# Kernel tuning notes

Measured on AMD Instinct MI355X. Metric: run time of the kernel, lower is better.

## Reference

```python
import jax, jax.numpy as jnp
import numpy as np

NEG_SLOPE = 0.2


def gat_conv(x, src, dst, W, a_src, a_dst, b, heads, out_ch, concat):
    """PyG-style GATConv (eval mode, self-loops already appended to src/dst)."""
    N = x.shape[0]
    h = (x @ W).reshape(N, heads, out_ch)            # [N,H,C]
    alpha_s = jnp.einsum('nhc,hc->nh', h, a_src)     # [N,H]
    alpha_d = jnp.einsum('nhc,hc->nh', h, a_dst)
    e = jax.nn.leaky_relu(alpha_s[src] + alpha_d[dst], NEG_SLOPE)  # [E,H]
    # segment softmax over incoming edges per destination node
    m = jax.ops.segment_max(e, dst, num_segments=N)  # every node has a self loop
    ex = jnp.exp(e - m[dst])
    denom = jax.ops.segment_sum(ex, dst, num_segments=N)
    alpha = ex / (denom[dst] + 1e-16)                # [E,H]
    msg = h[src] * alpha[:, :, None]                 # [E,H,C]
    out = jax.ops.segment_sum(msg, dst, num_segments=N)  # [N,H,C]
    if concat:
        out = out.reshape(N, heads * out_ch)
    else:
        out = out.mean(axis=1)
    return out + b


def setup_inputs() -> dict:
    key = jax.random.key(0)
    ks = jax.random.split(key, 12)
    N, E, F_IN = 100000, 3200000, 512
    H1, C1 = 8, 8           # conv1: heads=8, out=8, concat -> 64
    H2, C2 = 8, 16          # conv2: heads=8, out=num_classes=16, mean over heads
    x = jax.random.normal(ks[0], (N, F_IN), dtype=jnp.float32)
    edge_index = jax.random.randint(ks[1], (2, E), 0, N, dtype=jnp.int32)
    g = lambda k, s, fan: jax.random.normal(k, s, dtype=jnp.float32) / np.sqrt(fan)
    return {
        'x': x,
        'edge_index': edge_index,
        'W1': g(ks[2], (F_IN, H1 * C1), F_IN),
        'a_src1': g(ks[3], (H1, C1), C1),
        'a_dst1': g(ks[4], (H1, C1), C1),
        'b1': jnp.zeros((H1 * C1,), jnp.float32),
        'W2': g(ks[5], (H1 * C1, H2 * C2), H1 * C1),
        'a_src2': g(ks[6], (H2, C2), C2),
        'a_dst2': g(ks[7], (H2, C2), C2),
        'b2': jnp.zeros((C2,), jnp.float32),
    }


def reference(x, edge_index, W1, a_src1, a_dst1, b1, W2, a_src2, a_dst2, b2):
    N = x.shape[0]
    loops = jnp.arange(N, dtype=edge_index.dtype)
    src = jnp.concatenate([edge_index[0], loops])
    dst = jnp.concatenate([edge_index[1], loops])
    h = gat_conv(x, src, dst, W1, a_src1, a_dst1, b1, heads=8, out_ch=8, concat=True)
    h = jax.nn.elu(h)
    out = gat_conv(h, src, dst, W2, a_src2, a_dst2, b2, heads=8, out_ch=16, concat=False)
    return out
```

## Files before the change

kernel.cpp:

```cpp
#include <hip/hip_runtime.h>
#include <hip/hip_bf16.h>
#include <hip/hip_fp16.h>
#include <cstddef>

#define NEG_SLOPE 0.2f

typedef _Float16 half8 __attribute__((ext_vector_type(8)));
typedef float floatx4 __attribute__((ext_vector_type(4)));
typedef float floatx2 __attribute__((ext_vector_type(2)));


__global__ __launch_bounds__(256) void pre_k(const int* __restrict__ dst, int E,
                                             int* __restrict__ bhist, int* __restrict__ bh_blocks,
                                             int NB,
                                             const float* __restrict__ W1, _Float16* __restrict__ W1T,
                                             const float* __restrict__ W2, _Float16* __restrict__ W2T) {
    int b = blockIdx.x;
    if (b < 512) {
        __shared__ int lh[256];
        for (int t = threadIdx.x; t < 256; t += 256) lh[t] = 0;
        __syncthreads();
        int per = (E + 511) / 512;
        int s = b * per;
        int e = min(s + per, E);
        for (int i = s + threadIdx.x; i < e; i += 256) atomicAdd(&lh[dst[i] >> 9], 1);
        __syncthreads();
        for (int t = threadIdx.x; t < 256; t += 256) {
            int c = lh[t];
            bh_blocks[b * 256 + t] = c;
            if (c && t < NB) atomicAdd(&bhist[t], c);
        }
    } else if (b < 640) {
        int i = (b - 512) * 256 + threadIdx.x;
        if (i < 512 * 64) {
            int k = i / 64, n = i % 64;
            W1T[(size_t)n * 512 + k] = (_Float16)W1[i];
        }
    } else {
        int i = (b - 640) * 256 + threadIdx.x;
        if (i < 64 * 128) {
            int k = i / 128, n = i % 128;
            W2T[(size_t)n * 64 + k] = (_Float16)W2[i];
        }
    }
}

__global__ __launch_bounds__(256) void bucket_scan_k(const int* __restrict__ bhist, int NB,
                                                     int* __restrict__ bbase,
                                                     int* __restrict__ row_start, int N, int E) {
    __shared__ int tmp[256];
    int tid = threadIdx.x;
    int v = (tid < NB) ? bhist[tid] : 0;
    tmp[tid] = v;
    __syncthreads();
    for (int d = 1; d < 256; d <<= 1) {
        int t = tmp[tid];
        int a = (tid >= d) ? tmp[tid - d] : 0;
        __syncthreads();
        tmp[tid] = t + a;
        __syncthreads();
    }
    if (tid < NB) {
        bbase[tid] = tmp[tid] - v;
    }
    if (tid == 0) {
        bbase[NB] = E;
        row_start[N] = E;
    }
}

__global__ __launch_bounds__(256) void colscan_k(const int* __restrict__ bh_blocks,
                                                 const int* __restrict__ bbase,
                                                 int* __restrict__ pbase) {
    __shared__ int ssum[256];
    int t = blockIdx.x;
    int i = threadIdx.x;
    int v0 = bh_blocks[(2 * i) * 256 + t];
    int v1 = bh_blocks[(2 * i + 1) * 256 + t];
    int s = v0 + v1;
    ssum[i] = s;
    __syncthreads();
    for (int d = 1; d < 256; d <<= 1) {
        int x = ssum[i];
        int a = (i >= d) ? ssum[i - d] : 0;
        __syncthreads();
        ssum[i] = x + a;
        __syncthreads();
    }
    int excl = ssum[i] - s + bbase[t];
    pbase[(2 * i) * 256 + t] = excl;
    pbase[(2 * i + 1) * 256 + t] = excl + v0;
}

__global__ __launch_bounds__(256) void partition_k(const int* __restrict__ src,
                                                   const int* __restrict__ dst, int E,
                                                   const int* __restrict__ pbase,
                                                   unsigned int* __restrict__ part) {
    __shared__ int lbase[256];
    __shared__ int lh[256];
    int b = blockIdx.x;
    for (int t = threadIdx.x; t < 256; t += 256) {
        lbase[t] = pbase[b * 256 + t];
        lh[t] = 0;
    }
    __syncthreads();
    int per = (E + 511) / 512;
    int s = b * per;
    int e = min(s + per, E);
    for (int i = s + threadIdx.x; i < e; i += 256) {
        int d = dst[i];
        int bk = d >> 9;
        int lo = atomicAdd(&lh[bk], 1);
        part[lbase[bk] + lo] = ((unsigned)src[i] << 9) | (unsigned)(d & 511);
    }
}

__global__ __launch_bounds__(512) void bucket_build_k(const unsigned int* __restrict__ part,
                                                      const int* __restrict__ bbase,
                                                      int* __restrict__ row_start,
                                                      int* __restrict__ csr, int N) {
    __shared__ int cnt[512];
    __shared__ int cur[512];
    int b = blockIdx.x, tid = threadIdx.x;
    int n0 = b << 9;
    int s = bbase[b], e2 = bbase[b + 1];
    cnt[tid] = 0;
    __syncthreads();
    for (int i = s + tid; i < e2; i += 512) atomicAdd(&cnt[part[i] & 511], 1);
    __syncthreads();
    int v = cnt[tid];
    for (int d = 1; d < 512; d <<= 1) {
        int t = cnt[tid];
        int a = (tid >= d) ? cnt[tid - d] : 0;
        __syncthreads();
        cnt[tid] = t + a;
        __syncthreads();
    }
    int excl = cnt[tid] - v;
    if (n0 + tid < N) row_start[n0 + tid] = s + excl;
    cur[tid] = excl;
    __syncthreads();
    for (int i = s + tid; i < e2; i += 512) {
        unsigned u = part[i];
        int p = atomicAdd(&cur[u & 511], 1);
        csr[s + p] = (int)(u >> 9);
    }
}


__global__ __launch_bounds__(256) void gemm1_k(const float* __restrict__ A,
                                               const _Float16* __restrict__ BT,
                                               const float* __restrict__ a_s,
                                               const float* __restrict__ a_d,
                                               __half* __restrict__ C,
                                               float* __restrict__ os,
                                               float* __restrict__ od, int M) {
    constexpr int K = 512;
    __shared__ __align__(16) _Float16 Bs[2][64 * 64];
    int tid = threadIdx.x;
    int wave = tid >> 6, lane = tid & 63;
    int m16 = lane & 15, quad = lane >> 4;
    int row0 = blockIdx.x * 128 + wave * 32;
    int r0 = min(row0 + m16, M - 1);
    int r1 = min(row0 + 16 + m16, M - 1);
    const float* a0p = A + (size_t)r0 * K + quad * 8;
    const float* a1p = A + (size_t)r1 * K + quad * 8;

    int brow = tid >> 2;
    int bcb = tid & 3;
    const _Float16* bsrc = BT + (size_t)brow * K + bcb * 16;
    int du0 = ((bcb * 2 + 0) * 8) ^ ((brow & 7) << 3);
    int du1 = ((bcb * 2 + 1) * 8) ^ ((brow & 7) << 3);
    int dbase = brow * 64;

    floatx4 acc[2][4] = {};
    half8 b0 = *(const half8*)(bsrc + 0);
    half8 b1 = *(const half8*)(bsrc + 8);
    float4 a00 = *(const float4*)(a0p + 0);
    float4 a01 = *(const float4*)(a0p + 4);
    float4 a02 = *(const float4*)(a0p + 32);
    float4 a03 = *(const float4*)(a0p + 36);
    float4 a10 = *(const float4*)(a1p + 0);
    float4 a11 = *(const float4*)(a1p + 4);
    float4 a12 = *(const float4*)(a1p + 32);
    float4 a13 = *(const float4*)(a1p + 36);
    *(half8*)(&Bs[0][0] + dbase + du0) = b0;
    *(half8*)(&Bs[0][0] + dbase + du1) = b1;
    __syncthreads();

    int cur = 0;
    for (int s = 0; s < 8; ++s) {
        half8 af[2][2];
        af[0][0][0] = (_Float16)a00.x; af[0][0][1] = (_Float16)a00.y;
        af[0][0][2] = (_Float16)a00.z; af[0][0][3] = (_Float16)a00.w;
        af[0][0][4] = (_Float16)a01.x; af[0][0][5] = (_Float16)a01.y;
        af[0][0][6] = (_Float16)a01.z; af[0][0][7] = (_Float16)a01.w;
        af[0][1][0] = (_Float16)a02.x; af[0][1][1] = (_Float16)a02.y;
        af[0][1][2] = (_Float16)a02.z; af[0][1][3] = (_Float16)a02.w;
        af[0][1][4] = (_Float16)a03.x; af[0][1][5] = (_Float16)a03.y;
        af[0][1][6] = (_Float16)a03.z; af[0][1][7] = (_Float16)a03.w;
        af[1][0][0] = (_Float16)a10.x; af[1][0][1] = (_Float16)a10.y;
        af[1][0][2] = (_Float16)a10.z; af[1][0][3] = (_Float16)a10.w;
        af[1][0][4] = (_Float16)a11.x; af[1][0][5] = (_Float16)a11.y;
        af[1][0][6] = (_Float16)a11.z; af[1][0][7] = (_Float16)a11.w;
        af[1][1][0] = (_Float16)a12.x; af[1][1][1] = (_Float16)a12.y;
        af[1][1][2] = (_Float16)a12.z; af[1][1][3] = (_Float16)a12.w;
        af[1][1][4] = (_Float16)a13.x; af[1][1][5] = (_Float16)a13.y;
        af[1][1][6] = (_Float16)a13.z; af[1][1][7] = (_Float16)a13.w;
        if (s < 7) {
            int k1 = (s + 1) * 64;
            b0 = *(const half8*)(bsrc + k1);
            b1 = *(const half8*)(bsrc + k1 + 8);
            a00 = *(const float4*)(a0p + k1);
            a01 = *(const float4*)(a0p + k1 + 4);
            a02 = *(const float4*)(a0p + k1 + 32);
            a03 = *(const float4*)(a0p + k1 + 36);
            a10 = *(const float4*)(a1p + k1);
            a11 = *(const float4*)(a1p + k1 + 4);
            a12 = *(const float4*)(a1p + k1 + 32);
            a13 = *(const float4*)(a1p + k1 + 36);
        }
        const _Float16* bsC = &Bs[cur][0];
#pragma unroll
        for (int t = 0; t < 4; ++t) {
#pragma unroll
            for (int kk = 0; kk < 2; ++kk) {
                int idx = (t * 16 + m16) * 64 + ((kk * 32 + quad * 8) ^ ((m16 & 7) << 3));
                half8 bf = *(const half8*)(bsC + idx);
                acc[0][t] = __builtin_amdgcn_mfma_f32_16x16x32_f16(af[0][kk], bf, acc[0][t], 0, 0, 0);
                acc[1][t] = __builtin_amdgcn_mfma_f32_16x16x32_f16(af[1][kk], bf, acc[1][t], 0, 0, 0);
            }
        }
        if (s < 7) {
            _Float16* bsN = &Bs[cur ^ 1][0];
            *(half8*)(bsN + dbase + du0) = b0;
            *(half8*)(bsN + dbase + du1) = b1;
        }
        __syncthreads();
        cur ^= 1;
    }

    int head = (m16 >> 3);
#pragma unroll
    for (int rt = 0; rt < 2; ++rt) {
        int gmb = row0 + rt * 16 + quad * 4;
#pragma unroll
        for (int t = 0; t < 4; ++t) {
            float ws = a_s[(2 * t + head) * 8 + (m16 & 7)];
            float wd = a_d[(2 * t + head) * 8 + (m16 & 7)];
#pragma unroll
            for (int r = 0; r < 4; ++r) {
                int gm = gmb + r;
                float v = acc[rt][t][r];
                if (gm < M) C[(size_t)gm * 64 + t * 16 + m16] = __float2half(v);
                float sv = v * ws, dv = v * wd;
                sv += __shfl_xor(sv, 1, 64); dv += __shfl_xor(dv, 1, 64);
                sv += __shfl_xor(sv, 2, 64); dv += __shfl_xor(dv, 2, 64);
                sv += __shfl_xor(sv, 4, 64); dv += __shfl_xor(dv, 4, 64);
                if ((m16 & 7) == 0 && gm < M) {
                    os[gm * 8 + 2 * t + head] = sv;
                    od[gm * 8 + 2 * t + head] = dv;
                }
            }
        }
    }
}


__global__ __launch_bounds__(256) void gemm2_k(const _Float16* __restrict__ A,
                                               const _Float16* __restrict__ BT,
                                               const float* __restrict__ a_s,
                                               const float* __restrict__ a_d,
                                               unsigned short* __restrict__ Cf8,
                                               float* __restrict__ os,
                                               float* __restrict__ od, int M) {
    constexpr int NT = 8, K = 64;
    int wave = threadIdx.x >> 6, lane = threadIdx.x & 63;
    int m16 = lane & 15, quad = lane >> 4;
    int arow = blockIdx.x * 64 + wave * 16 + m16;
    int arc = arow < M ? arow : M - 1;
    floatx4 acc[NT] = {};
    for (int k0 = 0; k0 < K; k0 += 32) {
        half8 af = *(const half8*)(A + (size_t)arc * K + k0 + quad * 8);
#pragma unroll
        for (int t = 0; t < NT; ++t) {
            half8 bf = *(const half8*)(BT + (size_t)(t * 16 + m16) * K + k0 + quad * 8);
            acc[t] = __builtin_amdgcn_mfma_f32_16x16x32_f16(af, bf, acc[t], 0, 0, 0);
        }
    }
    int gm0 = blockIdx.x * 64 + wave * 16 + quad * 4;
#pragma unroll
    for (int t = 0; t < NT; ++t) {
        float ws = a_s[t * 16 + m16];
        float wd = a_d[t * 16 + m16];
#pragma unroll
        for (int r = 0; r < 4; ++r) {
            int gm = gm0 + r;
            float v = acc[t][r];
            float o = __shfl_xor(v, 1, 64);
            if (gm < M && !(m16 & 1)) {
                unsigned p = __builtin_amdgcn_cvt_pk_fp8_f32(v, o, 0, false);
                Cf8[(size_t)gm * 64 + t * 8 + (m16 >> 1)] = (unsigned short)(p & 0xffff);
            }
            float s = v * ws, d = v * wd;
            s += __shfl_xor(s, 1, 64); d += __shfl_xor(d, 1, 64);
            s += __shfl_xor(s, 2, 64); d += __shfl_xor(d, 2, 64);
            s += __shfl_xor(s, 4, 64); d += __shfl_xor(d, 4, 64);
            s += __shfl_xor(s, 8, 64); d += __shfl_xor(d, 8, 64);
            if (gm < M && m16 == t) {
                os[gm * 8 + t] = s;
                od[gm * 8 + t] = d;
            }
        }
    }
}


__global__ __launch_bounds__(256) void aggregate1_k(
    const uint2* __restrict__ H1, const float* __restrict__ as,
    const float* __restrict__ ad, const int* __restrict__ row_start,
    const int* __restrict__ csr, const float* __restrict__ b1,
    uint2* __restrict__ h1o, int N) {
    int l = threadIdx.x & 63;
    int wv = threadIdx.x >> 6;
    int ll = l & 31;
    int n = min((int)(blockIdx.x * 8 + wv * 2 + (l >> 5)), N - 1);
    int k = ll & 15;
    int jj = ll >> 4;
    int h = k >> 1;

    float adv = ad[n * 8 + h];
    float e0 = as[n * 8 + h] + adv;
    e0 = fmaxf(e0, NEG_SLOPE * e0);
    float ex0 = __expf(e0);
    float x0 = jj ? 0.f : ex0;

    uint2 sv = H1[(size_t)n * 16 + k];
    float2 s01 = __half22float2(*(const __half2*)&sv.x);
    float2 s23 = __half22float2(*(const __half2*)&sv.y);
    float denom = x0;
    float a0 = x0 * s01.x, a1 = x0 * s01.y, a2 = x0 * s23.x, a3 = x0 * s23.y;

    int e = row_start[n], end = row_start[n + 1];
    for (; e + 16 <= end; e += 16) {
        int sj[8];
        float xv[8];
#pragma unroll
        for (int u = 0; u < 8; ++u) sj[u] = csr[e + 2 * u + jj];
#pragma unroll
        for (int u = 0; u < 8; ++u) {
            float t = as[sj[u] * 8 + h] + adv;
            t = fmaxf(t, NEG_SLOPE * t);
            xv[u] = __expf(t);
        }
#pragma unroll
        for (int u = 0; u < 8; ++u) {
            uint2 gv = H1[(size_t)sj[u] * 16 + k];
            float2 v01 = __half22float2(*(const __half2*)&gv.x);
            float2 v23 = __half22float2(*(const __half2*)&gv.y);
            denom += xv[u];
            a0 = fmaf(xv[u], v01.x, a0); a1 = fmaf(xv[u], v01.y, a1);
            a2 = fmaf(xv[u], v23.x, a2); a3 = fmaf(xv[u], v23.y, a3);
        }
    }
    for (; e + 8 <= end; e += 8) {
#pragma unroll
        for (int u = 0; u < 4; ++u) {
            int sj = csr[e + 2 * u + jj];
            float t = as[sj * 8 + h] + adv;
            t = fmaxf(t, NEG_SLOPE * t);
            float x = __expf(t);
            uint2 gv = H1[(size_t)sj * 16 + k];
            float2 v01 = __half22float2(*(const __half2*)&gv.x);
            float2 v23 = __half22float2(*(const __half2*)&gv.y);
            denom += x;
            a0 = fmaf(x, v01.x, a0); a1 = fmaf(x, v01.y, a1);
            a2 = fmaf(x, v23.x, a2); a3 = fmaf(x, v23.y, a3);
        }
    }
    if (e < end) {
#pragma unroll
        for (int u = 0; u < 4; ++u) {
            int idx = e + 2 * u + jj;
            int sj = csr[min(idx, end - 1)];
            float t = as[sj * 8 + h] + adv;
            t = fmaxf(t, NEG_SLOPE * t);
            float x = idx < end ? __expf(t) : 0.f;
            uint2 gv = H1[(size_t)sj * 16 + k];
            float2 v01 = __half22float2(*(const __half2*)&gv.x);
            float2 v23 = __half22float2(*(const __half2*)&gv.y);
            denom += x;
            a0 = fmaf(x, v01.x, a0); a1 = fmaf(x, v01.y, a1);
            a2 = fmaf(x, v23.x, a2); a3 = fmaf(x, v23.y, a3);
        }
    }
    denom += __shfl_xor(denom, 16, 64);
    a0 += __shfl_xor(a0, 16, 64);
    a1 += __shfl_xor(a1, 16, 64);
    a2 += __shfl_xor(a2, 16, 64);
    a3 += __shfl_xor(a3, 16, 64);
    float inv = 1.f / denom;
    float r0 = a0 * inv + b1[4 * k + 0];
    float r1 = a1 * inv + b1[4 * k + 1];
    float r2 = a2 * inv + b1[4 * k + 2];
    float r3 = a3 * inv + b1[4 * k + 3];
    r0 = r0 > 0.f ? r0 : expm1f(r0);
    r1 = r1 > 0.f ? r1 : expm1f(r1);
    r2 = r2 > 0.f ? r2 : expm1f(r2);
    r3 = r3 > 0.f ? r3 : expm1f(r3);
    if (!jj) {
        __half2 p01 = __floats2half2_rn(r0, r1);
        __half2 p23 = __floats2half2_rn(r2, r3);
        uint2 o;
        o.x = *(const unsigned*)&p01;
        o.y = *(const unsigned*)&p23;
        h1o[(size_t)n * 16 + k] = o;
    }
}


__global__ __launch_bounds__(256) void aggregate2_k(
    const uint2* __restrict__ H2, const float* __restrict__ as,
    const float* __restrict__ ad, const int* __restrict__ row_start,
    const int* __restrict__ csr, const float* __restrict__ b2,
    float* __restrict__ out, int N) {
    int l = threadIdx.x & 63;
    int wv = threadIdx.x >> 6;
    int ll = l & 31;
    int n = min((int)(blockIdx.x * 8 + wv * 2 + (l >> 5)), N - 1);
    int k = ll & 15;
    int jj = ll >> 4;
    int h = k >> 1;

    float adv = ad[n * 8 + h];
    float e0 = as[n * 8 + h] + adv;
    e0 = fmaxf(e0, NEG_SLOPE * e0);
    float ex0 = __expf(e0);
    float x0 = jj ? 0.f : ex0;

    uint2 sv = H2[(size_t)n * 16 + k];
    floatx2 p01 = __builtin_amdgcn_cvt_pk_f32_fp8((int)sv.x, false);
    floatx2 p23 = __builtin_amdgcn_cvt_pk_f32_fp8((int)sv.x, true);
    floatx2 p45 = __builtin_amdgcn_cvt_pk_f32_fp8((int)sv.y, false);
    floatx2 p67 = __builtin_amdgcn_cvt_pk_f32_fp8((int)sv.y, true);
    float denom = x0;
    float a0 = x0 * p01[0], a1 = x0 * p01[1], a2 = x0 * p23[0], a3 = x0 * p23[1];
    float a4 = x0 * p45[0], a5 = x0 * p45[1], a6 = x0 * p67[0], a7 = x0 * p67[1];

    int e = row_start[n], end = row_start[n + 1];
    for (; e + 16 <= end; e += 16) {
        int sj[8];
        float xv[8];
#pragma unroll
        for (int u = 0; u < 8; ++u) sj[u] = csr[e + 2 * u + jj];
#pragma unroll
        for (int u = 0; u < 8; ++u) {
            float t = as[sj[u] * 8 + h] + adv;
            t = fmaxf(t, NEG_SLOPE * t);
            xv[u] = __expf(t);
        }
#pragma unroll
        for (int u = 0; u < 8; ++u) {
            uint2 gv = H2[(size_t)sj[u] * 16 + k];
            floatx2 v01 = __builtin_amdgcn_cvt_pk_f32_fp8((int)gv.x, false);
            floatx2 v23 = __builtin_amdgcn_cvt_pk_f32_fp8((int)gv.x, true);
            floatx2 v45 = __builtin_amdgcn_cvt_pk_f32_fp8((int)gv.y, false);
            floatx2 v67 = __builtin_amdgcn_cvt_pk_f32_fp8((int)gv.y, true);
            float x = xv[u];
            denom += x;
            a0 = fmaf(x, v01[0], a0); a1 = fmaf(x, v01[1], a1);
            a2 = fmaf(x, v23[0], a2); a3 = fmaf(x, v23[1], a3);
            a4 = fmaf(x, v45[0], a4); a5 = fmaf(x, v45[1], a5);
            a6 = fmaf(x, v67[0], a6); a7 = fmaf(x, v67[1], a7);
        }
    }
    for (; e + 8 <= end; e += 8) {
#pragma unroll
        for (int u = 0; u < 4; ++u) {
            int sj = csr[e + 2 * u + jj];
            float t = as[sj * 8 + h] + adv;
            t = fmaxf(t, NEG_SLOPE * t);
            float x = __expf(t);
            uint2 gv = H2[(size_t)sj * 16 + k];
            floatx2 v01 = __builtin_amdgcn_cvt_pk_f32_fp8((int)gv.x, false);
            floatx2 v23 = __builtin_amdgcn_cvt_pk_f32_fp8((int)gv.x, true);
            floatx2 v45 = __builtin_amdgcn_cvt_pk_f32_fp8((int)gv.y, false);
            floatx2 v67 = __builtin_amdgcn_cvt_pk_f32_fp8((int)gv.y, true);
            denom += x;
            a0 = fmaf(x, v01[0], a0); a1 = fmaf(x, v01[1], a1);
            a2 = fmaf(x, v23[0], a2); a3 = fmaf(x, v23[1], a3);
            a4 = fmaf(x, v45[0], a4); a5 = fmaf(x, v45[1], a5);
            a6 = fmaf(x, v67[0], a6); a7 = fmaf(x, v67[1], a7);
        }
    }
    if (e < end) {
#pragma unroll
        for (int u = 0; u < 4; ++u) {
            int idx = e + 2 * u + jj;
            int sj = csr[min(idx, end - 1)];
            float t = as[sj * 8 + h] + adv;
            t = fmaxf(t, NEG_SLOPE * t);
            float x = idx < end ? __expf(t) : 0.f;
            uint2 gv = H2[(size_t)sj * 16 + k];
            floatx2 v01 = __builtin_amdgcn_cvt_pk_f32_fp8((int)gv.x, false);
            floatx2 v23 = __builtin_amdgcn_cvt_pk_f32_fp8((int)gv.x, true);
            floatx2 v45 = __builtin_amdgcn_cvt_pk_f32_fp8((int)gv.y, false);
            floatx2 v67 = __builtin_amdgcn_cvt_pk_f32_fp8((int)gv.y, true);
            denom += x;
            a0 = fmaf(x, v01[0], a0); a1 = fmaf(x, v01[1], a1);
            a2 = fmaf(x, v23[0], a2); a3 = fmaf(x, v23[1], a3);
            a4 = fmaf(x, v45[0], a4); a5 = fmaf(x, v45[1], a5);
            a6 = fmaf(x, v67[0], a6); a7 = fmaf(x, v67[1], a7);
        }
    }
    denom += __shfl_xor(denom, 16, 64);
    float inv = 1.f / denom;
    a0 *= inv; a1 *= inv; a2 *= inv; a3 *= inv;
    a4 *= inv; a5 *= inv; a6 *= inv; a7 *= inv;
#pragma unroll
    for (int m = 2; m <= 16; m <<= 1) {
        a0 += __shfl_xor(a0, m, 64);
        a1 += __shfl_xor(a1, m, 64);
        a2 += __shfl_xor(a2, m, 64);
        a3 += __shfl_xor(a3, m, 64);
        a4 += __shfl_xor(a4, m, 64);
        a5 += __shfl_xor(a5, m, 64);
        a6 += __shfl_xor(a6, m, 64);
        a7 += __shfl_xor(a7, m, 64);
    }
    if (ll < 2) {
        int c0 = k * 8;
        float4 o0, o1;
        o0.x = a0 * 0.125f + b2[c0 + 0];
        o0.y = a1 * 0.125f + b2[c0 + 1];
        o0.z = a2 * 0.125f + b2[c0 + 2];
        o0.w = a3 * 0.125f + b2[c0 + 3];
        o1.x = a4 * 0.125f + b2[c0 + 4];
        o1.y = a5 * 0.125f + b2[c0 + 5];
        o1.z = a6 * 0.125f + b2[c0 + 6];
        o1.w = a7 * 0.125f + b2[c0 + 7];
        *(float4*)(out + (size_t)n * 16 + c0) = o0;
        *(float4*)(out + (size_t)n * 16 + c0 + 4) = o1;
    }
}


extern "C" void kernel_launch(void* const* d_in, const int* in_sizes, int n_in,
                              void* d_out, int out_size, void* d_ws, size_t ws_size,
                              hipStream_t stream) {
    (void)n_in; (void)out_size; (void)ws_size;
    const float* x      = (const float*)d_in[0];
    const int*   ei     = (const int*)d_in[1];
    const float* W1     = (const float*)d_in[2];
    const float* a_src1 = (const float*)d_in[3];
    const float* a_dst1 = (const float*)d_in[4];
    const float* b1     = (const float*)d_in[5];
    const float* W2     = (const float*)d_in[6];
    const float* a_src2 = (const float*)d_in[7];
    const float* a_dst2 = (const float*)d_in[8];
    const float* b2     = (const float*)d_in[9];

    int N = in_sizes[0] / 512;
    int E = in_sizes[1] / 2;
    const int* src = ei;
    const int* dst = ei + E;
    int NB = (N + 511) >> 9;

    char* ws = (char*)d_ws;
    size_t off = 0;
    auto alloc = [&](size_t bytes) -> void* {
        void* p = ws + off;
        off = (off + bytes + 255) & ~(size_t)255;
        return p;
    };
    __half* h1  = (__half*)alloc((size_t)N * 64 * 2);
    __half* h1o = (__half*)alloc((size_t)N * 64 * 2);
    unsigned short* h2f8 = (unsigned short*)alloc((size_t)N * 64 * 2);
    float* as1  = (float*)alloc((size_t)N * 8 * 4);
    float* ad1  = (float*)alloc((size_t)N * 8 * 4);
    float* as2  = (float*)alloc((size_t)N * 8 * 4);
    float* ad2  = (float*)alloc((size_t)N * 8 * 4);
    _Float16* W1T = (_Float16*)alloc((size_t)512 * 64 * 2);
    _Float16* W2T = (_Float16*)alloc((size_t)64 * 128 * 2);
    int* row_start = (int*)alloc((size_t)(N + 1) * 4);
    int* bhist     = (int*)alloc(256 * 4);
    int* bbase     = (int*)alloc(257 * 4);
    int* bh_blocks = (int*)alloc((size_t)512 * 256 * 4);
    int* pbase     = (int*)alloc((size_t)512 * 256 * 4);
    unsigned int* part = (unsigned int*)alloc((size_t)E * 4);
    int* csr       = (int*)alloc((size_t)E * 4);

    hipMemsetAsync(bhist, 0, 256 * 4, stream);
    pre_k<<<672, 256, 0, stream>>>(dst, E, bhist, bh_blocks, NB, W1, W1T, W2, W2T);
    bucket_scan_k<<<1, 256, 0, stream>>>(bhist, NB, bbase, row_start, N, E);
    colscan_k<<<NB, 256, 0, stream>>>(bh_blocks, bbase, pbase);
    partition_k<<<512, 256, 0, stream>>>(src, dst, E, pbase, part);
    bucket_build_k<<<NB, 512, 0, stream>>>(part, bbase, row_start, csr, N);

    int g1blocks = (N + 127) / 128;
    int g2blocks = (N + 63) / 64;
    int ablocks  = (N + 7) / 8;

    gemm1_k<<<g1blocks, 256, 0, stream>>>(x, W1T, a_src1, a_dst1, h1, as1, ad1, N);
    aggregate1_k<<<ablocks, 256, 0, stream>>>((const uint2*)h1, as1, ad1, row_start,
                                              csr, b1, (uint2*)h1o, N);

    gemm2_k<<<g2blocks, 256, 0, stream>>>((const _Float16*)h1o, W2T, a_src2, a_dst2,
                                          h2f8, as2, ad2, N);
    aggregate2_k<<<ablocks, 256, 0, stream>>>((const uint2*)h2f8, as2, ad2,
                                              row_start, csr, b2, (float*)d_out, N);
}
```

Baseline: 626.8 us.

## Merge scan kernels, fuse partition with GEMM1, prefetch aggregation loads, packed conversions

Folds the bucket scan and column scan into one launch by making the column scan produce bucket-relative offsets and adding bbase later in the partition step. The partition pass and GEMM1 now run as one heterogeneous grid so the memory-bound scatter can overlap with the compute-bound GEMM. The two aggregation kernels prefetch the next batch of CSR indices and issue attention and feature gathers up front for more memory-level parallelism. GEMM1 switches its fp32-to-fp16 conversion to packed round-toward-zero instructions, which changes rounding slightly and raises register pressure.

Result: faster. 610.4 us (-2.6%).

```diff
diff --git a/kernel.cpp b/kernel.cpp
--- a/kernel.cpp
+++ b/kernel.cpp
@@ -6,8 +6,11 @@
 #define NEG_SLOPE 0.2f
 
 typedef _Float16 half8 __attribute__((ext_vector_type(8)));
+typedef __fp16 fp16x2 __attribute__((ext_vector_type(2)));
 typedef float floatx4 __attribute__((ext_vector_type(4)));
 typedef float floatx2 __attribute__((ext_vector_type(2)));
+
+union H8 { half8 v; fp16x2 p[4]; };
 
 
 __global__ __launch_bounds__(256) void pre_k(const int* __restrict__ dst, int E,
@@ -45,73 +48,45 @@
     }
 }
 
-__global__ __launch_bounds__(256) void bucket_scan_k(const int* __restrict__ bhist, int NB,
-                                                     int* __restrict__ bbase,
-                                                     int* __restrict__ row_start, int N, int E) {
+__global__ __launch_bounds__(256) void scan2_k(const int* __restrict__ bhist, int NB,
+                                               const int* __restrict__ bh_blocks,
+                                               int* __restrict__ bbase, int* __restrict__ row_start,
+                                               int* __restrict__ pbase, int N, int E) {
     __shared__ int tmp[256];
     int tid = threadIdx.x;
-    int v = (tid < NB) ? bhist[tid] : 0;
-    tmp[tid] = v;
-    __syncthreads();
-    for (int d = 1; d < 256; d <<= 1) {
-        int t = tmp[tid];
-        int a = (tid >= d) ? tmp[tid - d] : 0;
-        __syncthreads();
-        tmp[tid] = t + a;
-        __syncthreads();
-    }
-    if (tid < NB) {
-        bbase[tid] = tmp[tid] - v;
-    }
-    if (tid == 0) {
-        bbase[NB] = E;
-        row_start[N] = E;
-    }
-}
-
-__global__ __launch_bounds__(256) void colscan_k(const int* __restrict__ bh_blocks,
-                                                 const int* __restrict__ bbase,
-                                                 int* __restrict__ pbase) {
-    __shared__ int ssum[256];
-    int t = blockIdx.x;
-    int i = threadIdx.x;
-    int v0 = bh_blocks[(2 * i) * 256 + t];
-    int v1 = bh_blocks[(2 * i + 1) * 256 + t];
-    int s = v0 + v1;
-    ssum[i] = s;
-    __syncthreads();
-    for (int d = 1; d < 256; d <<= 1) {
-        int x = ssum[i];
-        int a = (i >= d) ? ssum[i - d] : 0;
-        __syncthreads();
-        ssum[i] = x + a;
-        __syncthreads();
-    }
-    int excl = ssum[i] - s + bbase[t];
-    pbase[(2 * i) * 256 + t] = excl;
-    pbase[(2 * i + 1) * 256 + t] = excl + v0;
-}
-
-__global__ __launch_bounds__(256) void partition_k(const int* __restrict__ src,
-                                                   const int* __restrict__ dst, int E,
-                                                   const int* __restrict__ pbase,
-                                                   unsigned int* __restrict__ part) {
-    __shared__ int lbase[256];
-    __shared__ int lh[256];
-    int b = blockIdx.x;
-    for (int t = threadIdx.x; t < 256; t += 256) {
-        lbase[t] = pbase[b * 256 + t];
-        lh[t] = 0;
-    }
-    __syncthreads();
-    int per = (E + 511) / 512;
-    int s = b * per;
-    int e = min(s + per, E);
-    for (int i = s + threadIdx.x; i < e; i += 256) {
-        int d = dst[i];
-        int bk = d >> 9;
-        int lo = atomicAdd(&lh[bk], 1);
-        part[lbase[bk] + lo] = ((unsigned)src[i] << 9) | (unsigned)(d & 511);
+    if (blockIdx.x == 0) {
+        int v = (tid < NB) ? bhist[tid] : 0;
+        tmp[tid] = v;
+        __syncthreads();
+        for (int d = 1; d < 256; d <<= 1) {
+            int t = tmp[tid];
+            int a = (tid >= d) ? tmp[tid - d] : 0;
+            __syncthreads();
+            tmp[tid] = t + a;
+            __syncthreads();
+        }
+        if (tid < NB) bbase[tid] = tmp[tid] - v;
+        if (tid == 0) {
+            bbase[NB] = E;
+            row_start[N] = E;
+        }
+    } else {
+        int t = blockIdx.x - 1;
+        int v0 = bh_blocks[(2 * tid) * 256 + t];
+        int v1 = bh_blocks[(2 * tid + 1) * 256 + t];
+        int s = v0 + v1;
+        tmp[tid] = s;
+        __syncthreads();
+        for (int d = 1; d < 256; d <<= 1) {
+            int x = tmp[tid];
+            int a = (tid >= d) ? tmp[tid - d] : 0;
+            __syncthreads();
+            tmp[tid] = x + a;
+            __syncthreads();
+        }
+        int excl = tmp[tid] - s;
+        pbase[(2 * tid) * 256 + t] = excl;
+        pbase[(2 * tid + 1) * 256 + t] = excl + v0;
     }
 }
 
@@ -148,19 +123,42 @@
 }
 
 
-__global__ __launch_bounds__(256) void gemm1_k(const float* __restrict__ A,
-                                               const _Float16* __restrict__ BT,
-                                               const float* __restrict__ a_s,
-                                               const float* __restrict__ a_d,
-                                               __half* __restrict__ C,
-                                               float* __restrict__ os,
-                                               float* __restrict__ od, int M) {
+__global__ __launch_bounds__(256) void part_gemm1_k(
+    const float* __restrict__ A, const _Float16* __restrict__ BT,
+    const float* __restrict__ a_s, const float* __restrict__ a_d,
+    __half* __restrict__ C, float* __restrict__ os, float* __restrict__ od, int M,
+    const int* __restrict__ src, const int* __restrict__ dst, int E,
+    const int* __restrict__ bbase, const int* __restrict__ pbase,
+    unsigned int* __restrict__ part) {
+    __shared__ __align__(16) _Float16 Bs[2][64 * 64];
+    __shared__ int lbase[256];
+    __shared__ int lh[256];
+
+    if (blockIdx.x < 512) {
+        int b = blockIdx.x;
+        for (int t = threadIdx.x; t < 256; t += 256) {
+            lbase[t] = bbase[t] + pbase[b * 256 + t];
+            lh[t] = 0;
+        }
+        __syncthreads();
+        int per = (E + 511) / 512;
+        int s = b * per;
+        int e = min(s + per, E);
+        for (int i = s + threadIdx.x; i < e; i += 256) {
+            int d = dst[i];
+            int bk = d >> 9;
+            int lo = atomicAdd(&lh[bk], 1);
+            part[lbase[bk] + lo] = ((unsigned)src[i] << 9) | (unsigned)(d & 511);
+        }
+        return;
+    }
+
     constexpr int K = 512;
-    __shared__ __align__(16) _Float16 Bs[2][64 * 64];
+    int bid = blockIdx.x - 512;
     int tid = threadIdx.x;
     int wave = tid >> 6, lane = tid & 63;
     int m16 = lane & 15, quad = lane >> 4;
-    int row0 = blockIdx.x * 128 + wave * 32;
+    int row0 = bid * 128 + wave * 32;
     int r0 = min(row0 + m16, M - 1);
     int r1 = min(row0 + 16 + m16, M - 1);
     const float* a0p = A + (size_t)r0 * K + quad * 8;
@@ -191,22 +189,27 @@
     int cur = 0;
     for (int s = 0; s < 8; ++s) {
         half8 af[2][2];
-        af[0][0][0] = (_Float16)a00.x; af[0][0][1] = (_Float16)a00.y;
-        af[0][0][2] = (_Float16)a00.z; af[0][0][3] = (_Float16)a00.w;
-        af[0][0][4] = (_Float16)a01.x; af[0][0][5] = (_Float16)a01.y;
-        af[0][0][6] = (_Float16)a01.z; af[0][0][7] = (_Float16)a01.w;
-        af[0][1][0] = (_Float16)a02.x; af[0][1][1] = (_Float16)a02.y;
-        af[0][1][2] = (_Float16)a02.z; af[0][1][3] = (_Float16)a02.w;
-        af[0][1][4] = (_Float16)a03.x; af[0][1][5] = (_Float16)a03.y;
-        af[0][1][6] = (_Float16)a03.z; af[0][1][7] = (_Float16)a03.w;
-        af[1][0][0] = (_Float16)a10.x; af[1][0][1] = (_Float16)a10.y;
-        af[1][0][2] = (_Float16)a10.z; af[1][0][3] = (_Float16)a10.w;
-        af[1][0][4] = (_Float16)a11.x; af[1][0][5] = (_Float16)a11.y;
-        af[1][0][6] = (_Float16)a11.z; af[1][0][7] = (_Float16)a11.w;
-        af[1][1][0] = (_Float16)a12.x; af[1][1][1] = (_Float16)a12.y;
-        af[1][1][2] = (_Float16)a12.z; af[1][1][3] = (_Float16)a12.w;
-        af[1][1][4] = (_Float16)a13.x; af[1][1][5] = (_Float16)a13.y;
-        af[1][1][6] = (_Float16)a13.z; af[1][1][7] = (_Float16)a13.w;
+        H8 u;
+        u.p[0] = __builtin_amdgcn_cvt_pkrtz(a00.x, a00.y);
+        u.p[1] = __builtin_amdgcn_cvt_pkrtz(a00.z, a00.w);
+        u.p[2] = __builtin_amdgcn_cvt_pkrtz(a01.x, a01.y);
+        u.p[3] = __builtin_amdgcn_cvt_pkrtz(a01.z, a01.w);
+        af[0][0] = u.v;
+        u.p[0] = __builtin_amdgcn_cvt_pkrtz(a02.x, a02.y);
+        u.p[1] = __builtin_amdgcn_cvt_pkrtz(a02.z, a02.w);
+        u.p[2] = __builtin_amdgcn_cvt_pkrtz(a03.x, a03.y);
+        u.p[3] = __builtin_amdgcn_cvt_pkrtz(a03.z, a03.w);
+        af[0][1] = u.v;
+        u.p[0] = __builtin_amdgcn_cvt_pkrtz(a10.x, a10.y);
+        u.p[1] = __builtin_amdgcn_cvt_pkrtz(a10.z, a10.w);
+        u.p[2] = __builtin_amdgcn_cvt_pkrtz(a11.x, a11.y);
+        u.p[3] = __builtin_amdgcn_cvt_pkrtz(a11.z, a11.w);
+        af[1][0] = u.v;
+        u.p[0] = __builtin_amdgcn_cvt_pkrtz(a12.x, a12.y);
+        u.p[1] = __builtin_amdgcn_cvt_pkrtz(a12.z, a12.w);
+        u.p[2] = __builtin_amdgcn_cvt_pkrtz(a13.x, a13.y);
+        u.p[3] = __builtin_amdgcn_cvt_pkrtz(a13.z, a13.w);
+        af[1][1] = u.v;
         if (s < 7) {
             int k1 = (s + 1) * 64;
             b0 = *(const half8*)(bsrc + k1);
@@ -329,6 +332,13 @@
     int jj = ll >> 4;
     int h = k >> 1;
 
+    int e = row_start[n], end = row_start[n + 1];
+    int sjA[8];
+    if (e + 16 <= end) {
+#pragma unroll
+        for (int u = 0; u < 8; ++u) sjA[u] = csr[e + 2 * u + jj];
+    }
+
     float adv = ad[n * 8 + h];
     float e0 = as[n * 8 + h] + adv;
     e0 = fmaxf(e0, NEG_SLOPE * e0);
@@ -341,27 +351,34 @@
     float denom = x0;
     float a0 = x0 * s01.x, a1 = x0 * s01.y, a2 = x0 * s23.x, a3 = x0 * s23.y;
 
-    int e = row_start[n], end = row_start[n + 1];
     for (; e + 16 <= end; e += 16) {
-        int sj[8];
+        bool hasNext = (e + 32 <= end);
+        float tA[8];
+        int sjN[8];
+        uint2 gv[8];
+#pragma unroll
+        for (int u = 0; u < 8; ++u) tA[u] = as[sjA[u] * 8 + h];
+#pragma unroll
+        for (int u = 0; u < 8; ++u) sjN[u] = hasNext ? csr[e + 16 + 2 * u + jj] : sjA[u];
+#pragma unroll
+        for (int u = 0; u < 8; ++u) gv[u] = H1[(size_t)sjA[u] * 16 + k];
         float xv[8];
 #pragma unroll
-        for (int u = 0; u < 8; ++u) sj[u] = csr[e + 2 * u + jj];
-#pragma unroll
         for (int u = 0; u < 8; ++u) {
-            float t = as[sj[u] * 8 + h] + adv;
+            float t = tA[u] + adv;
             t = fmaxf(t, NEG_SLOPE * t);
             xv[u] = __expf(t);
         }
 #pragma unroll
         for (int u = 0; u < 8; ++u) {
-            uint2 gv = H1[(size_t)sj[u] * 16 + k];
-            float2 v01 = __half22float2(*(const __half2*)&gv.x);
-            float2 v23 = __half22float2(*(const __half2*)&gv.y);
+            float2 v01 = __half22float2(*(const __half2*)&gv[u].x);
+            float2 v23 = __half22float2(*(const __half2*)&gv[u].y);
             denom += xv[u];
             a0 = fmaf(xv[u], v01.x, a0); a1 = fmaf(xv[u], v01.y, a1);
             a2 = fmaf(xv[u], v23.x, a2); a3 = fmaf(xv[u], v23.y, a3);
         }
+#pragma unroll
+        for (int u = 0; u < 8; ++u) sjA[u] = sjN[u];
     }
     for (; e + 8 <= end; e += 8) {
 #pragma unroll
@@ -432,6 +449,13 @@
     int jj = ll >> 4;
     int h = k >> 1;
 
+    int e = row_start[n], end = row_start[n + 1];
+    int sjA[8];
+    if (e + 16 <= end) {
+#pragma unroll
+        for (int u = 0; u < 8; ++u) sjA[u] = csr[e + 2 * u + jj];
+    }
+
     float adv = ad[n * 8 + h];
     float e0 = as[n * 8 + h] + adv;
     e0 = fmaxf(e0, NEG_SLOPE * e0);
@@ -447,25 +471,30 @@
     float a0 = x0 * p01[0], a1 = x0 * p01[1], a2 = x0 * p23[0], a3 = x0 * p23[1];
     float a4 = x0 * p45[0], a5 = x0 * p45[1], a6 = x0 * p67[0], a7 = x0 * p67[1];
 
-    int e = row_start[n], end = row_start[n + 1];
     for (; e + 16 <= end; e += 16) {
-        int sj[8];
+        bool hasNext = (e + 32 <= end);
+        float tA[8];
+        int sjN[8];
+        uint2 gv[8];
+#pragma unroll
+        for (int u = 0; u < 8; ++u) tA[u] = as[sjA[u] * 8 + h];
+#pragma unroll
+        for (int u = 0; u < 8; ++u) sjN[u] = hasNext ? csr[e + 16 + 2 * u + jj] : sjA[u];
+#pragma unroll
+        for (int u = 0; u < 8; ++u) gv[u] = H2[(size_t)sjA[u] * 16 + k];
         float xv[8];
 #pragma unroll
-        for (int u = 0; u < 8; ++u) sj[u] = csr[e + 2 * u + jj];
-#pragma unroll
         for (int u = 0; u < 8; ++u) {
-            float t = as[sj[u] * 8 + h] + adv;
+            float t = tA[u] + adv;
             t = fmaxf(t, NEG_SLOPE * t);
             xv[u] = __expf(t);
         }
 #pragma unroll
         for (int u = 0; u < 8; ++u) {
-            uint2 gv = H2[(size_t)sj[u] * 16 + k];
-            floatx2 v01 = __builtin_amdgcn_cvt_pk_f32_fp8((int)gv.x, false);
-            floatx2 v23 = __builtin_amdgcn_cvt_pk_f32_fp8((int)gv.x, true);
-            floatx2 v45 = __builtin_amdgcn_cvt_pk_f32_fp8((int)gv.y, false);
-            floatx2 v67 = __builtin_amdgcn_cvt_pk_f32_fp8((int)gv.y, true);
+            floatx2 v01 = __builtin_amdgcn_cvt_pk_f32_fp8((int)gv[u].x, false);
+            floatx2 v23 = __builtin_amdgcn_cvt_pk_f32_fp8((int)gv[u].x, true);
+            floatx2 v45 = __builtin_amdgcn_cvt_pk_f32_fp8((int)gv[u].y, false);
+            floatx2 v67 = __builtin_amdgcn_cvt_pk_f32_fp8((int)gv[u].y, true);
             float x = xv[u];
             denom += x;
             a0 = fmaf(x, v01[0], a0); a1 = fmaf(x, v01[1], a1);
@@ -473,6 +502,8 @@
             a4 = fmaf(x, v45[0], a4); a5 = fmaf(x, v45[1], a5);
             a6 = fmaf(x, v67[0], a6); a7 = fmaf(x, v67[1], a7);
         }
+#pragma unroll
+        for (int u = 0; u < 8; ++u) sjA[u] = sjN[u];
     }
     for (; e + 8 <= end; e += 8) {
 #pragma unroll
@@ -590,18 +621,17 @@
     unsigned int* part = (unsigned int*)alloc((size_t)E * 4);
     int* csr       = (int*)alloc((size_t)E * 4);
 
-    hipMemsetAsync(bhist, 0, 256 * 4, stream);
-    pre_k<<<672, 256, 0, stream>>>(dst, E, bhist, bh_blocks, NB, W1, W1T, W2, W2T);
-    bucket_scan_k<<<1, 256, 0, stream>>>(bhist, NB, bbase, row_start, N, E);
-    colscan_k<<<NB, 256, 0, stream>>>(bh_blocks, bbase, pbase);
-    partition_k<<<512, 256, 0, stream>>>(src, dst, E, pbase, part);
-    bucket_build_k<<<NB, 512, 0, stream>>>(part, bbase, row_start, csr, N);
-
     int g1blocks = (N + 127) / 128;
     int g2blocks = (N + 63) / 64;
     int ablocks  = (N + 7) / 8;
 
-    gemm1_k<<<g1blocks, 256, 0, stream>>>(x, W1T, a_src1, a_dst1, h1, as1, ad1, N);
+    hipMemsetAsync(bhist, 0, 256 * 4, stream);
+    pre_k<<<672, 256, 0, stream>>>(dst, E, bhist, bh_blocks, NB, W1, W1T, W2, W2T);
+    scan2_k<<<1 + NB, 256, 0, stream>>>(bhist, NB, bh_blocks, bbase, row_start, pbase, N, E);
+    part_gemm1_k<<<512 + g1blocks, 256, 0, stream>>>(x, W1T, a_src1, a_dst1, h1, as1, ad1, N,
+                                                     src, dst, E, bbase, pbase, part);
+    bucket_build_k<<<NB, 512, 0, stream>>>(part, bbase, row_start, csr, N);
+
     aggregate1_k<<<ablocks, 256, 0, stream>>>((const uint2*)h1, as1, ad1, row_start,
                                               csr, b1, (uint2*)h1o, N);
 
```
